# Performance work log

Measured on AMD Instinct MI355X. Metric: run time of the kernel, lower is better.

The kernel has to match this reference:

```python
import jax, jax.numpy as jnp
import numpy as np


def lrelu(x):
    return jax.nn.leaky_relu(x, 0.1)


def mask_softmax(a, mask, axis=-1):
    # faithful to the torch version: max over ALL entries, mask applied post-exp
    a_max = jnp.max(a, axis=axis, keepdims=True)
    e = jnp.exp(a - a_max) * mask
    return e / (jnp.sum(e, axis=axis, keepdims=True) + 1e-6)


def gru_cell(x, h, w_ih, w_hh, b_ih, b_hh):
    # torch.nn.GRUCell math; weights stored as [in, 3H]
    gi = x @ w_ih + b_ih
    gh = h @ w_hh + b_hh
    ir, iz, inn = jnp.split(gi, 3, axis=-1)
    hr, hz, hn = jnp.split(gh, 3, axis=-1)
    r = jax.nn.sigmoid(ir + hr)
    z = jax.nn.sigmoid(iz + hz)
    n = jnp.tanh(inn + r * hn)
    return (1 - z) * n + z * h


def setup_inputs() -> dict:
    key = jax.random.key(0)
    B, N, M, E, H, D, K = 128, 256, 12, 256, 128, 3, 2
    AF, BF, NA, NB = 82, 6, 100, 12
    ks = iter(jax.random.split(key, 64))
    nrm = lambda shape: jax.random.normal(next(ks), shape, jnp.float32) * 0.05
    return dict(
        batch_size=B,
        vertex_mask=jnp.ones((B, N), jnp.float32),
        vertex=jax.random.randint(next(ks), (B, N), 0, NA, dtype=jnp.int32),
        edge=jax.random.randint(next(ks), (B, E), 0, NB, dtype=jnp.int32),
        atom_adj=jax.random.randint(next(ks), (B * N * M,), 0, B * N, dtype=jnp.int32),
        bond_adj=jax.random.randint(next(ks), (B * N * M,), 0, B * E, dtype=jnp.int32),
        nbs_mask=jnp.ones((B, N, M), jnp.float32),
        init_atom_features=nrm((NA, AF)),
        init_bond_features=nrm((NB, BF)),
        emb_w=nrm((AF, H)), emb_b=nrm((H,)),
        Wa_main_w=nrm((D, K, H, H)), Wa_main_b=nrm((D, K, H)),
        Wbmm_w=nrm((D, K, H)), Wbmm_b=nrm((D, K)),
        Wmain_w=nrm((D, K, H, H)), Wmain_b=nrm((D, K, H)),
        Wm2s_w=nrm((D, K * H, H)), Wm2s_b=nrm((D, H)),
        Ws2m_w=nrm((D, H, H)), Ws2m_b=nrm((D, H)),
        Wsuper_w=nrm((D, H, H)), Wsuper_b=nrm((D, H)),
        Wzm1_w=nrm((D, H, H)), Wzm1_b=nrm((D, H)),
        Wzm2_w=nrm((D, H, H)), Wzm2_b=nrm((D, H)),
        Wzs1_w=nrm((D, H, H)), Wzs1_b=nrm((D, H)),
        Wzs2_w=nrm((D, H, H)), Wzs2_b=nrm((D, H)),
        U2_w=nrm((D, H + BF, H)), U2_b=nrm((D, H)),
        U1_w=nrm((D, 2 * H, H)), U1_b=nrm((D, H)),
        gm_wih=nrm((H, 3 * H)), gm_whh=nrm((H, 3 * H)), gm_bih=nrm((3 * H,)), gm_bhh=nrm((3 * H,)),
        gs_wih=nrm((H, 3 * H)), gs_whh=nrm((H, 3 * H)), gs_bih=nrm((3 * H,)), gs_bhh=nrm((3 * H,)),
    )


def reference(batch_size, vertex_mask, vertex, edge, atom_adj, bond_adj, nbs_mask,
              init_atom_features, init_bond_features, emb_w, emb_b,
              Wa_main_w, Wa_main_b, Wbmm_w, Wbmm_b, Wmain_w, Wmain_b,
              Wm2s_w, Wm2s_b, Ws2m_w, Ws2m_b, Wsuper_w, Wsuper_b,
              Wzm1_w, Wzm1_b, Wzm2_w, Wzm2_b, Wzs1_w, Wzs1_b, Wzs2_w, Wzs2_b,
              U2_w, U2_b, U1_w, U1_b,
              gm_wih, gm_whh, gm_bih, gm_bhh, gs_wih, gs_whh, gs_bih, gs_bhh):
    B = batch_size
    N = vertex_mask.shape[1]
    M = nbs_mask.shape[2]
    H = emb_w.shape[1]
    BF = init_bond_features.shape[1]
    D, K = Wa_main_w.shape[0], Wa_main_w.shape[1]

    vertex_initial = init_atom_features[vertex]          # [B,N,AF]
    edge_initial = init_bond_features[edge]              # [B,E,BF]
    vf = lrelu(vertex_initial @ emb_w + emb_b)           # [B,N,H]
    vm = vertex_mask[:, :, None]
    sf = jnp.sum(vf * vm, axis=1, keepdims=True)         # [B,1,H] super node

    for d in range(D):
        # multi-head super-node attention (all k heads vectorized)
        a_main = jnp.tanh(jnp.einsum('bnh,khg->bkng', vf, Wa_main_w[d]) + Wa_main_b[d][None, :, None, :])
        a = jnp.einsum('bkng,kg->bkn', a_main * sf[:, None, :, :], Wbmm_w[d]) + Wbmm_b[d][None, :, None]
        attn = mask_softmax(a, vertex_mask[:, None, :])                  # [B,K,N]
        wv = jnp.einsum('bnh,khg->bkng', vf, Wmain_w[d]) + Wmain_b[d][None, :, None, :]
        m = jnp.einsum('bkn,bkng->bkg', attn, wv).reshape(B, 1, K * H)   # head-concat
        main_to_super = jnp.tanh(m @ Wm2s_w[d] + Wm2s_b[d])              # [B,1,H]

        # WLN unit: gather neighbor atom/bond features, fused MLP + masked sum
        vnei = vf.reshape(-1, H)[atom_adj].reshape(B, N, M, H)
        enei = edge_initial.reshape(-1, BF)[bond_adj].reshape(B, N, M, BF)
        nei = jnp.concatenate([vnei, enei], axis=-1)                     # [B,N,M,H+BF]
        nei_label = lrelu(nei @ U2_w[d] + U2_b[d])
        nei_label = jnp.sum(nei_label * nbs_mask[..., None], axis=-2)    # [B,N,H]
        main_self = lrelu(jnp.concatenate([vf, nei_label], axis=-1) @ U1_w[d] + U1_b[d])

        super_to_main = jnp.tanh(sf @ Ws2m_w[d] + Ws2m_b[d])
        super_self = jnp.tanh(sf @ Wsuper_w[d] + Wsuper_b[d])

        z_main = jax.nn.sigmoid(main_self @ Wzm1_w[d] + Wzm1_b[d]
                                + super_to_main @ Wzm2_w[d] + Wzm2_b[d])
        hidden_main = (1 - z_main) * main_self + z_main * super_to_main
        vf = gru_cell(hidden_main.reshape(-1, H), vf.reshape(-1, H),
                      gm_wih, gm_whh, gm_bih, gm_bhh).reshape(B, N, H)

        z_super = jax.nn.sigmoid(super_self @ Wzs1_w[d] + Wzs1_b[d]
                                 + main_to_super @ Wzs2_w[d] + Wzs2_b[d])
        hidden_super = (1 - z_super) * super_self + z_super * main_to_super
        sf = gru_cell(hidden_super.reshape(B, H), sf.reshape(B, H),
                      gs_wih, gs_whh, gs_bih, gs_bhh).reshape(B, 1, H)

    return (vf, sf)
```

## Files before the change

kernel.cpp:

```cpp
#include <hip/hip_runtime.h>

typedef unsigned short ushort_t;
typedef unsigned int uint_t;
typedef unsigned char uchar_t;
typedef __attribute__((ext_vector_type(8))) short short8;
typedef __attribute__((ext_vector_type(4))) float f32x4;
typedef __attribute__((ext_vector_type(2))) float f32x2;

#define B   128
#define Nv  256
#define Mn  12
#define Hd  128
#define Dd  3
#define Kk  2
#define AFd 82
#define BFd 6
#define BN  (B*Nv)

enum { EPI_NONE = 0, EPI_LRELU = 1 };

__device__ __forceinline__ float lrelu(float x) { return fmaxf(x, 0.1f * x); }
__device__ __forceinline__ float sigmoidf(float x) { return 1.f / (1.f + expf(-x)); }
__device__ __forceinline__ ushort_t f2b(float x) {
    uint_t u = __float_as_uint(x);
    return (ushort_t)((u + 0x7FFFu + ((u >> 16) & 1u)) >> 16);
}
__device__ __forceinline__ float b2f(ushort_t s) {
    return __uint_as_float(((uint_t)s) << 16);
}
__device__ __forceinline__ void b2f4(uint2 u, float* o) {
    o[0] = __uint_as_float((u.x & 0xFFFFu) << 16);
    o[1] = __uint_as_float(u.x & 0xFFFF0000u);
    o[2] = __uint_as_float((u.y & 0xFFFFu) << 16);
    o[3] = __uint_as_float(u.y & 0xFFFF0000u);
}
__device__ __forceinline__ uint_t pk2(float lo, float hi) {
    return (uint_t)f2b(lo) | ((uint_t)f2b(hi) << 16);
}
__device__ __forceinline__ float upk_lo(uint_t u) { return __uint_as_float((u & 0xFFFFu) << 16); }
__device__ __forceinline__ float upk_hi(uint_t u) { return __uint_as_float(u & 0xFFFF0000u); }
__device__ __forceinline__ uchar_t f2e8(float x) {
    return (uchar_t)(__builtin_amdgcn_cvt_pk_fp8_f32(x, 0.f, 0, false) & 0xFF);
}

struct PrepJob {
    const float* W;
    long sliceStride;
    int K, ldw, nPerSlice, Kspan, KpadRow, kDst, total, outOff, blockStart;
};
struct PrepJobs { PrepJob j[18]; int nJobs; };

__global__ __launch_bounds__(256) void k_prep_all(PrepJobs P, ushort_t* __restrict__ WT)
{
    int bid = blockIdx.x;
    int ji = 0;
    #pragma unroll 1
    while (ji + 1 < P.nJobs && P.j[ji + 1].blockStart <= bid) ++ji;
    const PrepJob J = P.j[ji];
    const int idx = (bid - J.blockStart) * 256 + threadIdx.x;
    if (idx >= J.total) return;
    const int n = idx / J.Kspan, k = idx % J.Kspan;
    const int slice = n / J.nPerSlice, nn = n % J.nPerSlice;
    float v = (k < J.K) ? J.W[(size_t)slice * J.sliceStride + (size_t)k * J.ldw + nn] : 0.f;
    WT[(size_t)J.outOff + (size_t)n * J.KpadRow + J.kDst + k] = f2b(v);
}

__global__ __launch_bounds__(256) void k_qtab(const float* __restrict__ init_bond,
                                              const float* __restrict__ U2w,
                                              ushort_t* __restrict__ qt)
{
    const int d = blockIdx.x;
    const float* W = U2w + (size_t)d * (Hd + BFd) * Hd + (size_t)Hd * Hd;
    ushort_t* q = qt + (size_t)d * 12 * Hd;
    for (int idx = threadIdx.x; idx < 12 * Hd; idx += 256) {
        const int j = idx >> 7, h = idx & 127;
        float s = 0.f;
        #pragma unroll
        for (int f = 0; f < BFd; ++f) s += init_bond[j * BFd + f] * W[f * Hd + h];
        q[idx] = f2b(s);
    }
}

template<int EPI, bool ABF, bool OBF>
__global__ __launch_bounds__(256) void mgemm(
    const void* __restrict__ A1v, int lda1, int K1,
    const int* __restrict__ rowidx,
    const ushort_t* __restrict__ Wt, int Kpad,
    const float* __restrict__ b1,
    void* __restrict__ outv, long ldo)
{
    const int t    = threadIdx.x;
    const int lane = t & 63;
    const int w    = t >> 6;
    const int wm   = w >> 1, wn = w & 1;
    const int lr   = lane & 15, lg = lane >> 4;
    const int row0 = blockIdx.x * 64;

    __shared__ ushort_t As[64 * 64];

    f32x4 acc[2][4];
    #pragma unroll
    for (int i = 0; i < 2; ++i)
        #pragma unroll
        for (int j = 0; j < 4; ++j)
            acc[i][j] = (f32x4){0.f, 0.f, 0.f, 0.f};

    const int r_st = t >> 2, q4 = t & 3;
    const int grow = row0 + r_st;
    const long arow = rowidx ? (long)rowidx[grow] : (long)grow;

    const int nck = Kpad >> 6;
    for (int ck = 0; ck < nck; ++ck) {
        if (ck) __syncthreads();
        {
            const int kb = ck * 64 + q4 * 16;
            union { ushort_t us[16]; uint4 qv[2]; } tmp;
            #pragma unroll
            for (int j = 0; j < 16; ++j) {
                const int kg = kb + j;
                ushort_t v = 0;
                if (kg < K1) {
                    if (ABF) v = ((const ushort_t*)A1v)[(size_t)arow * lda1 + kg];
                    else     v = f2b(((const float*)A1v)[(size_t)arow * lda1 + kg]);
                }
                tmp.us[j] = v;
            }
            #pragma unroll
            for (int j = 0; j < 2; ++j) {
                int byte = r_st * 128 + q4 * 32 + j * 16;
                byte ^= ((r_st & 7) << 4);
                *(uint4*)((char*)As + byte) = tmp.qv[j];
            }
        }
        __syncthreads();
        #pragma unroll
        for (int ks = 0; ks < 64; ks += 32) {
            short8 af[2], bfr[4];
            #pragma unroll
            for (int mf = 0; mf < 2; ++mf) {
                const int row = wm * 32 + mf * 16 + lr;
                int byte = row * 128 + (ks + lg * 8) * 2;
                byte ^= ((row & 7) << 4);
                af[mf] = *(const short8*)((const char*)As + byte);
            }
            #pragma unroll
            for (int nf = 0; nf < 4; ++nf) {
                const int col = wn * 64 + nf * 16 + lr;
                bfr[nf] = *(const short8*)(Wt + (size_t)col * Kpad + ck * 64 + ks + lg * 8);
            }
            #pragma unroll
            for (int mf = 0; mf < 2; ++mf)
                #pragma unroll
                for (int nf = 0; nf < 4; ++nf)
                    acc[mf][nf] = __builtin_amdgcn_mfma_f32_16x16x32_bf16(
                        af[mf], bfr[nf], acc[mf][nf], 0, 0, 0);
        }
    }

    #pragma unroll
    for (int mf = 0; mf < 2; ++mf) {
        #pragma unroll
        for (int nf = 0; nf < 4; ++nf) {
            const int c = wn * 64 + nf * 16 + lr;
            #pragma unroll
            for (int reg = 0; reg < 4; ++reg) {
                const int r = wm * 32 + mf * 16 + lg * 4 + reg;
                const size_t row = (size_t)row0 + r;
                float v = acc[mf][nf][reg];
                if (b1) v += b1[c];
                if constexpr (EPI == EPI_LRELU) v = lrelu(v);
                const size_t oidx = row * ldo + c;
                if (OBF) ((ushort_t*)outv)[oidx] = f2b(v);
                else     ((float*)outv)[oidx] = v;
            }
        }
    }
}

__global__ __launch_bounds__(256) void k_tdp(
    const ushort_t* __restrict__ vfb,
    const ushort_t* __restrict__ Wt,
    const float* __restrict__ waB,
    const float* __restrict__ u2B,
    const float* __restrict__ sf,
    const float* __restrict__ wbmmW,
    const float* __restrict__ wbmmB,
    float* __restrict__ a_out,
    uchar_t* __restrict__ Pout)
{
    const int t = threadIdx.x;
    const int lane = t & 63, w = t >> 6;
    const int wm = w >> 1, wn = w & 1;
    const int lr = lane & 15, lg = lane >> 4;
    const int row0 = blockIdx.x * 64;
    const int ky = blockIdx.y;
    const int b = row0 >> 8;

    __shared__ ushort_t As[64 * 128];
    __shared__ float EUs[128], EBb[128];
    __shared__ float red[64][2];

    {
        const int r_st = t >> 2, q4 = t & 3;
        const ushort_t* src = vfb + (size_t)(row0 + r_st) * Hd + q4 * 32;
        #pragma unroll
        for (int j = 0; j < 4; ++j) {
            uint4 v = ((const uint4*)src)[j];
            int byte = r_st * 256 + q4 * 64 + j * 16;
            byte ^= ((r_st & 7) << 4);
            *(uint4*)((char*)As + byte) = v;
        }
    }
    if (ky != 2 && t < 128) {
        EUs[t] = sf[b * Hd + t] * wbmmW[ky * Hd + t];
        EBb[t] = waB[ky * Hd + t];
    }
    __syncthreads();

    const ushort_t* Wty = Wt + (size_t)ky * 16384;

    f32x4 acc[2][4];
    #pragma unroll
    for (int i = 0; i < 2; ++i)
        #pragma unroll
        for (int j = 0; j < 4; ++j)
            acc[i][j] = (f32x4){0.f, 0.f, 0.f, 0.f};

    #pragma unroll
    for (int kk = 0; kk < 128; kk += 32) {
        short8 af[2], bfr[4];
        #pragma unroll
        for (int nf = 0; nf < 4; ++nf) {
            const int col = wn * 64 + nf * 16 + lr;
            bfr[nf] = *(const short8*)(Wty + (size_t)col * 128 + kk + lg * 8);
        }
        #pragma unroll
        for (int mf = 0; mf < 2; ++mf) {
            const int row = wm * 32 + mf * 16 + lr;
            int byte = row * 256 + (kk + lg * 8) * 2;
            byte ^= ((row & 7) << 4);
            af[mf] = *(const short8*)((const char*)As + byte);
        }
        #pragma unroll
        for (int mf = 0; mf < 2; ++mf)
            #pragma unroll
            for (int nf = 0; nf < 4; ++nf)
                acc[mf][nf] = __builtin_amdgcn_mfma_f32_16x16x32_bf16(
                    af[mf], bfr[nf], acc[mf][nf], 0, 0, 0);
    }

    if (ky == 2) {
        #pragma unroll
        for (int mf = 0; mf < 2; ++mf)
            #pragma unroll
            for (int nf = 0; nf < 4; ++nf) {
                const int c = wn * 64 + nf * 16 + lr;
                #pragma unroll
                for (int reg = 0; reg < 4; ++reg) {
                    const int r = wm * 32 + mf * 16 + lg * 4 + reg;
                    Pout[(size_t)(row0 + r) * Hd + c] = f2e8(acc[mf][nf][reg] + u2B[c]);
                }
            }
    } else {
        #pragma unroll
        for (int mf = 0; mf < 2; ++mf) {
            #pragma unroll
            for (int reg = 0; reg < 4; ++reg) {
                float p = 0.f;
                #pragma unroll
                for (int nf = 0; nf < 4; ++nf) {
                    const int c = wn * 64 + nf * 16 + lr;
                    p += tanhf(acc[mf][nf][reg] + EBb[c]) * EUs[c];
                }
                p += __shfl_xor(p, 1); p += __shfl_xor(p, 2);
                p += __shfl_xor(p, 4); p += __shfl_xor(p, 8);
                if (lr == 0) red[wm * 32 + mf * 16 + lg * 4 + reg][wn] = p;
            }
        }
        __syncthreads();
        if (t < 64) {
            const int gr = row0 + t;
            a_out[(size_t)(gr >> 8) * 512 + (size_t)ky * 256 + (gr & 255)] =
                red[t][0] + red[t][1] + wbmmB[ky];
        }
    }
}

__device__ __forceinline__ void gemv1(const float* __restrict__ W0, const float* __restrict__ x0,
                                      int ldw, int off, int K,
                                      float (*red)[8][32][4],
                                      float* __restrict__ y0, int t)
{
    const int gq = t & 31, hs = t >> 5;
    const int hn = K >> 3;
    f32x4 a0 = (f32x4){0.f,0.f,0.f,0.f};
    const float* Wp0 = W0 + off + (size_t)gq * 4;
    const int h0 = hs * hn;
    #pragma unroll 8
    for (int i = 0; i < hn; ++i) {
        const float4 w0 = *(const float4*)&Wp0[(size_t)(h0 + i) * ldw];
        const float v0 = x0[h0 + i];
        a0.x = fmaf(v0, w0.x, a0.x); a0.y = fmaf(v0, w0.y, a0.y);
        a0.z = fmaf(v0, w0.z, a0.z); a0.w = fmaf(v0, w0.w, a0.w);
    }
    *(f32x4*)&red[0][hs][gq][0] = a0;
    __syncthreads();
    if (t < 128) {
        float s0 = 0.f;
        #pragma unroll
        for (int p = 0; p < 8; ++p) s0 += red[0][p][t >> 2][t & 3];
        y0[t] = s0;
    }
    __syncthreads();
}

__device__ __forceinline__ void gemv2(const float* __restrict__ W0, const float* __restrict__ x0,
                                      const float* __restrict__ W1, const float* __restrict__ x1,
                                      int ldw, int off, int K,
                                      float (*red)[8][32][4],
                                      float* __restrict__ y0, float* __restrict__ y1, int t)
{
    const int gq = t & 31, hs = t >> 5;
    const int hn = K >> 3;
    f32x4 a0 = (f32x4){0.f,0.f,0.f,0.f}, a1 = (f32x4){0.f,0.f,0.f,0.f};
    const float* Wp0 = W0 + off + (size_t)gq * 4;
    const float* Wp1 = W1 + off + (size_t)gq * 4;
    const int h0 = hs * hn;
    #pragma unroll 4
    for (int i = 0; i < hn; ++i) {
        const float4 w0 = *(const float4*)&Wp0[(size_t)(h0 + i) * ldw];
        const float4 w1 = *(const float4*)&Wp1[(size_t)(h0 + i) * ldw];
        const float v0 = x0[h0 + i], v1 = x1[h0 + i];
        a0.x = fmaf(v0, w0.x, a0.x); a0.y = fmaf(v0, w0.y, a0.y);
        a0.z = fmaf(v0, w0.z, a0.z); a0.w = fmaf(v0, w0.w, a0.w);
        a1.x = fmaf(v1, w1.x, a1.x); a1.y = fmaf(v1, w1.y, a1.y);
        a1.z = fmaf(v1, w1.z, a1.z); a1.w = fmaf(v1, w1.w, a1.w);
    }
    *(f32x4*)&red[0][hs][gq][0] = a0;
    *(f32x4*)&red[1][hs][gq][0] = a1;
    __syncthreads();
    if (t < 128) {
        float s0 = 0.f, s1 = 0.f;
        #pragma unroll
        for (int p = 0; p < 8; ++p) {
            s0 += red[0][p][t >> 2][t & 3];
            s1 += red[1][p][t >> 2][t & 3];
        }
        y0[t] = s0; y1[t] = s1;
    }
    __syncthreads();
}

__device__ __forceinline__ void gemv3(const float* __restrict__ W0, const float* __restrict__ x0,
                                      const float* __restrict__ W1, const float* __restrict__ x1,
                                      const float* __restrict__ W2, const float* __restrict__ x2,
                                      int ldw, int off, int K,
                                      float (*red)[8][32][4],
                                      float* __restrict__ y0, float* __restrict__ y1,
                                      float* __restrict__ y2, int t)
{
    const int gq = t & 31, hs = t >> 5;
    const int hn = K >> 3;
    f32x4 a0 = (f32x4){0.f,0.f,0.f,0.f}, a1 = (f32x4){0.f,0.f,0.f,0.f}, a2 = (f32x4){0.f,0.f,0.f,0.f};
    const float* Wp0 = W0 + off + (size_t)gq * 4;
    const float* Wp1 = W1 + off + (size_t)gq * 4;
    const float* Wp2 = W2 + off + (size_t)gq * 4;
    const int h0 = hs * hn;
    #pragma unroll 4
    for (int i = 0; i < hn; ++i) {
        const float4 w0 = *(const float4*)&Wp0[(size_t)(h0 + i) * ldw];
        const float4 w1 = *(const float4*)&Wp1[(size_t)(h0 + i) * ldw];
        const float4 w2 = *(const float4*)&Wp2[(size_t)(h0 + i) * ldw];
        const float v0 = x0[h0 + i], v1 = x1[h0 + i], v2 = x2[h0 + i];
        a0.x = fmaf(v0, w0.x, a0.x); a0.y = fmaf(v0, w0.y, a0.y);
        a0.z = fmaf(v0, w0.z, a0.z); a0.w = fmaf(v0, w0.w, a0.w);
        a1.x = fmaf(v1, w1.x, a1.x); a1.y = fmaf(v1, w1.y, a1.y);
        a1.z = fmaf(v1, w1.z, a1.z); a1.w = fmaf(v1, w1.w, a1.w);
        a2.x = fmaf(v2, w2.x, a2.x); a2.y = fmaf(v2, w2.y, a2.y);
        a2.z = fmaf(v2, w2.z, a2.z); a2.w = fmaf(v2, w2.w, a2.w);
    }
    *(f32x4*)&red[0][hs][gq][0] = a0;
    *(f32x4*)&red[1][hs][gq][0] = a1;
    *(f32x4*)&red[2][hs][gq][0] = a2;
    __syncthreads();
    if (t < 128) {
        float s0 = 0.f, s1 = 0.f, s2 = 0.f;
        #pragma unroll
        for (int p = 0; p < 8; ++p) {
            s0 += red[0][p][t >> 2][t & 3];
            s1 += red[1][p][t >> 2][t & 3];
            s2 += red[2][p][t >> 2][t & 3];
        }
        y0[t] = s0; y1[t] = s1; y2[t] = s2;
    }
    __syncthreads();
}

__global__ __launch_bounds__(256) void k_gsup(
    const float* __restrict__ a_buf, const float* __restrict__ vmask,
    const ushort_t* __restrict__ vfb,
    const float* __restrict__ sf_in,
    const float* __restrict__ Wm, const float* __restrict__ bm,
    const float* __restrict__ Wm2s, const float* __restrict__ bm2s,
    const float* __restrict__ Ws2m, const float* __restrict__ bs2m,
    const float* __restrict__ Wsup, const float* __restrict__ bsup,
    const float* __restrict__ Wzm2, const float* __restrict__ bzm2,
    const float* __restrict__ Wzs1, const float* __restrict__ bzs1,
    const float* __restrict__ Wzs2, const float* __restrict__ bzs2,
    const float* __restrict__ gwih, const float* __restrict__ gwhh,
    const float* __restrict__ gbih, const float* __restrict__ gbhh,
    float* __restrict__ s2m_g, float* __restrict__ czm2_g,
    float* __restrict__ sf_out,
    const uchar_t* __restrict__ P8, const ushort_t* __restrict__ qt,
    const int* __restrict__ aadj, const int* __restrict__ badj,
    const int* __restrict__ edge, const float* __restrict__ nmask,
    ushort_t* __restrict__ nei)
{
    const int t = threadIdx.x;

    if (blockIdx.x >= B) {
        __shared__ ushort_t aiS[64 * Mn];
        __shared__ ushort_t eiS[64 * Mn];
        __shared__ ushort_t mkS[64 * Mn];
        const int row0 = (blockIdx.x - B) * 64;
        for (int i = t; i < 64 * Mn; i += 256) {
            const int r = i / Mn, m = i - r * Mn;
            const long g = (long)(row0 + r) * Mn + m;
            aiS[i] = (ushort_t)aadj[g];
            eiS[i] = (ushort_t)edge[badj[g]];
            mkS[i] = f2b(nmask[g]);
        }
        __syncthreads();
        #pragma unroll 1
        for (int it = 0; it < 4; ++it) {
            const int idx = it * 256 + t;
            const int r = idx >> 4, h0 = (idx & 15) * 8;
            float a8[8] = {0.f,0.f,0.f,0.f,0.f,0.f,0.f,0.f};
            #pragma unroll
            for (int m = 0; m < Mn; ++m) {
                const int ai = aiS[r * Mn + m];
                const float mk = b2f(mkS[r * Mn + m]);
                const uint2 pv = *(const uint2*)&P8[(size_t)ai * Hd + h0];
                const uint4 qv = *(const uint4*)&qt[(size_t)eiS[r * Mn + m] * Hd + h0];
                const f32x2 p01 = __builtin_amdgcn_cvt_pk_f32_fp8((int)pv.x, false);
                const f32x2 p23 = __builtin_amdgcn_cvt_pk_f32_fp8((int)pv.x, true);
                const f32x2 p45 = __builtin_amdgcn_cvt_pk_f32_fp8((int)pv.y, false);
                const f32x2 p67 = __builtin_amdgcn_cvt_pk_f32_fp8((int)pv.y, true);
                const float pf[8] = {p01[0], p01[1], p23[0], p23[1], p45[0], p45[1], p67[0], p67[1]};
                const ushort_t* qq = (const ushort_t*)&qv;
                #pragma unroll
                for (int e = 0; e < 8; ++e) {
                    const float v = pf[e] + b2f(qq[e]);
                    a8[e] = fmaf(mk, lrelu(v), a8[e]);
                }
            }
            ushort_t o8[8];
            #pragma unroll
            for (int e = 0; e < 8; ++e) o8[e] = f2b(a8[e]);
            *(uint4*)&nei[(size_t)(row0 + r) * Hd + h0] = *(const uint4*)o8;
        }
        return;
    }

    const int b = blockIdx.x;
    const int wid = t >> 6, lane = t & 63;
    __shared__ float red[3][8][32][4];
    __shared__ float att0[256], att1[256];
    __shared__ float sfl[128], tbA[128], tbB[128], mv[256];
    __shared__ float ms2[128], s2ml[128], ssl[128], hsl[128];
    __shared__ float tmp1[128], tmp2[128], tmp3[128];
    __shared__ float gib[384], ghb[384];
    __shared__ float saS[2];
    __shared__ float lm[4][2], ls[4][2];

    const float v0 = a_buf[(size_t)b * 512 + t];
    const float v1 = a_buf[(size_t)b * 512 + 256 + t];
    const float vm = vmask[b * Nv + t];
    float m0 = v0, m1 = v1;
    #pragma unroll
    for (int o = 1; o < 64; o <<= 1) {
        m0 = fmaxf(m0, __shfl_xor(m0, o));
        m1 = fmaxf(m1, __shfl_xor(m1, o));
    }
    if (lane == 0) { lm[wid][0] = m0; lm[wid][1] = m1; }
    __syncthreads();
    m0 = fmaxf(fmaxf(lm[0][0], lm[1][0]), fmaxf(lm[2][0], lm[3][0]));
    m1 = fmaxf(fmaxf(lm[0][1], lm[1][1]), fmaxf(lm[2][1], lm[3][1]));
    const float e0v = expf(v0 - m0) * vm;
    const float e1v = expf(v1 - m1) * vm;
    float s0 = e0v, s1 = e1v;
    #pragma unroll
    for (int o = 1; o < 64; o <<= 1) {
        s0 += __shfl_xor(s0, o);
        s1 += __shfl_xor(s1, o);
    }
    if (lane == 0) { ls[wid][0] = s0; ls[wid][1] = s1; }
    if (t < 128) sfl[t] = sf_in[b * Hd + t];
    __syncthreads();
    s0 = ls[0][0] + ls[1][0] + ls[2][0] + ls[3][0];
    s1 = ls[0][1] + ls[1][1] + ls[2][1] + ls[3][1];
    att0[t] = e0v / (s0 + 1e-6f);
    att1[t] = e1v / (s1 + 1e-6f);
    if (t == 0) { saS[0] = s0 / (s0 + 1e-6f); saS[1] = s1 / (s1 + 1e-6f); }
    __syncthreads();

    {
        const int hq = t & 31, ns = t >> 5;
        f32x4 a0 = (f32x4){0.f,0.f,0.f,0.f}, a1 = (f32x4){0.f,0.f,0.f,0.f};
        const ushort_t* base = vfb + (size_t)b * Nv * Hd + hq * 4;
        #pragma unroll 8
        for (int i = 0; i < 32; ++i) {
            const int n = ns * 32 + i;
            float xv[4];
            b2f4(*(const uint2*)&base[(size_t)n * Hd], xv);
            const float w0 = att0[n], w1 = att1[n];
            a0.x = fmaf(w0, xv[0], a0.x); a0.y = fmaf(w0, xv[1], a0.y);
            a0.z = fmaf(w0, xv[2], a0.z); a0.w = fmaf(w0, xv[3], a0.w);
            a1.x = fmaf(w1, xv[0], a1.x); a1.y = fmaf(w1, xv[1], a1.y);
            a1.z = fmaf(w1, xv[2], a1.z); a1.w = fmaf(w1, xv[3], a1.w);
        }
        *(f32x4*)&red[0][ns][hq][0] = a0;
        *(f32x4*)&red[1][ns][hq][0] = a1;
        __syncthreads();
        if (t < 128) {
            float u0 = 0.f, u1 = 0.f;
            #pragma unroll
            for (int p = 0; p < 8; ++p) {
                u0 += red[0][p][t >> 2][t & 3];
                u1 += red[1][p][t >> 2][t & 3];
            }
            tbA[t] = u0; tbB[t] = u1;
        }
        __syncthreads();
    }

    gemv2(Wm, tbA, Wm + Hd * Hd, tbB, Hd, 0, Hd, red, mv, mv + 128, t);
    mv[t] += saS[t >> 7] * bm[t];
    __syncthreads();

    gemv1(Wm2s, mv, Hd, 0, 2 * Hd, red, tmp1, t);
    if (t < 128) ms2[t] = tanhf(tmp1[t] + bm2s[t]);
    __syncthreads();

    gemv2(Ws2m, sfl, Wsup, sfl, Hd, 0, Hd, red, tmp1, tmp2, t);
    if (t < 128) {
        const float v = tanhf(tmp1[t] + bs2m[t]);
        s2ml[t] = v; s2m_g[b * Hd + t] = v;
        ssl[t] = tanhf(tmp2[t] + bsup[t]);
    }
    __syncthreads();

    gemv3(Wzm2, s2ml, Wzs1, ssl, Wzs2, ms2, Hd, 0, Hd, red, tmp1, tmp2, tmp3, t);
    if (t < 128) {
        czm2_g[b * Hd + t] = tmp1[t] + bzm2[t];
        const float zs = sigmoidf(tmp2[t] + bzs1[t] + tmp3[t] + bzs2[t]);
        hsl[t] = (1.f - zs) * ssl[t] + zs * ms2[t];
    }
    __syncthreads();

    #pragma unroll 1
    for (int c = 0; c < 3; ++c)
        gemv2(gwih, hsl, gwhh, sfl, 3 * Hd, c * Hd, Hd, red, gib + c * Hd, ghb + c * Hd, t);
    if (t < 128) {
        const float r = sigmoidf(gib[t] + gbih[t] + ghb[t] + gbhh[t]);
        const float z = sigmoidf(gib[128 + t] + gbih[128 + t] + ghb[128 + t] + gbhh[128 + t]);
        const float n = tanhf(gib[256 + t] + gbih[256 + t] + r * (ghb[256 + t] + gbhh[256 + t]));
        sf_out[b * Hd + t] = (1.f - z) * n + z * sfl[t];
    }
}

__global__ __launch_bounds__(256) void k_mega(
    const ushort_t* __restrict__ vfb,
    const ushort_t* __restrict__ nei,
    const ushort_t* __restrict__ wt_u1,
    const ushort_t* __restrict__ wt_zm1,
    const ushort_t* __restrict__ wt_rz,
    const ushort_t* __restrict__ wt_inn,
    const ushort_t* __restrict__ wt_hn,
    const float* __restrict__ u1b,
    const float* __restrict__ zm1b,
    const float* __restrict__ bih, const float* __restrict__ bhh,
    const float* __restrict__ czm2, const float* __restrict__ s2m,
    void* __restrict__ outv, const int finalFp32)
{
    const int t = threadIdx.x;
    const int lane = t & 63;
    const int wn = t >> 6;
    const int lr = lane & 15, lg = lane >> 4;
    const int row0 = blockIdx.x * 32;
    const int b = row0 >> 8;

    __shared__ ushort_t As[32 * 256];

    {
        const int r_st = t >> 3, q8 = t & 7;
        const ushort_t* srcV = vfb + (size_t)(row0 + r_st) * Hd + q8 * 16;
        const ushort_t* srcN = nei + (size_t)(row0 + r_st) * Hd + q8 * 16;
        uint4 v0 = ((const uint4*)srcV)[0];
        uint4 v1 = ((const uint4*)srcV)[1];
        uint4 n0 = ((const uint4*)srcN)[0];
        uint4 n1 = ((const uint4*)srcN)[1];
        int bV0 = (r_st * 512 + q8 * 32)            ^ ((r_st & 7) << 4);
        int bV1 = (r_st * 512 + q8 * 32 + 16)       ^ ((r_st & 7) << 4);
        int bN0 = (r_st * 512 + 256 + q8 * 32)      ^ ((r_st & 7) << 4);
        int bN1 = (r_st * 512 + 256 + q8 * 32 + 16) ^ ((r_st & 7) << 4);
        *(uint4*)((char*)As + bV0) = v0;
        *(uint4*)((char*)As + bV1) = v1;
        *(uint4*)((char*)As + bN0) = n0;
        *(uint4*)((char*)As + bN1) = n1;
    }
    __syncthreads();

    f32x4 acc[2][2];

#define ZERO_ACC2() { _Pragma("unroll") for (int i = 0; i < 2; ++i) _Pragma("unroll") for (int j = 0; j < 2; ++j) acc[i][j] = (f32x4){0.f,0.f,0.f,0.f}; }
#define AF_L32(LC) (*(const short8*)((const char*)As + ((((mf * 16 + lr) * 512 + ((LC) + lg * 8) * 2)) ^ ((lr & 7) << 4))))
#define GEMM_PASS32(WG, KPADW, KTOT, A_EXPR) { \
        ZERO_ACC2(); \
        _Pragma("unroll") \
        for (int kk = 0; kk < (KTOT); kk += 32) { \
            short8 af[2], bfv[2]; \
            _Pragma("unroll") \
            for (int nf = 0; nf < 2; ++nf) \
                bfv[nf] = *(const short8*)((WG) + (size_t)(wn * 32 + nf * 16 + lr) * (KPADW) + kk + lg * 8); \
            _Pragma("unroll") \
            for (int mf = 0; mf < 2; ++mf) \
                af[mf] = (A_EXPR); \
            _Pragma("unroll") \
            for (int mf = 0; mf < 2; ++mf) \
                _Pragma("unroll") \
                for (int nf = 0; nf < 2; ++nf) \
                    acc[mf][nf] = __builtin_amdgcn_mfma_f32_16x16x32_bf16(af[mf], bfv[nf], acc[mf][nf], 0, 0, 0); \
        } }

    GEMM_PASS32(wt_u1, 256, 256, AF_L32(kk));
    {
        uint_t msp[2][2][2];
        #pragma unroll
        for (int mf = 0; mf < 2; ++mf)
            #pragma unroll
            for (int nf = 0; nf < 2; ++nf) {
                const int c = wn * 32 + nf * 16 + lr;
                const float bb = u1b[c];
                msp[mf][nf][0] = pk2(lrelu(acc[mf][nf][0] + bb), lrelu(acc[mf][nf][1] + bb));
                msp[mf][nf][1] = pk2(lrelu(acc[mf][nf][2] + bb), lrelu(acc[mf][nf][3] + bb));
            }
        __syncthreads();
        #pragma unroll
        for (int mf = 0; mf < 2; ++mf)
            #pragma unroll
            for (int nf = 0; nf < 2; ++nf) {
                const int c = wn * 32 + nf * 16 + lr;
                #pragma unroll
                for (int reg = 0; reg < 4; ++reg) {
                    const int row = mf * 16 + lg * 4 + reg;
                    const uint_t pk = msp[mf][nf][reg >> 1];
                    const ushort_t msb = (reg & 1) ? (ushort_t)(pk >> 16) : (ushort_t)(pk & 0xFFFFu);
                    int byte = row * 512 + (128 + c) * 2;
                    byte ^= ((row & 7) << 4);
                    *(ushort_t*)((char*)As + byte) = msb;
                }
            }
    }
    __syncthreads();

    GEMM_PASS32(wt_zm1, 128, 128, AF_L32(128 + kk));
    {
        uint_t zpk[2][2][2];
        #pragma unroll
        for (int mf = 0; mf < 2; ++mf)
            #pragma unroll
            for (int nf = 0; nf < 2; ++nf) {
                const int c = wn * 32 + nf * 16 + lr;
                const float bb = zm1b[c] + czm2[b * Hd + c];
                zpk[mf][nf][0] = pk2(sigmoidf(acc[mf][nf][0] + bb), sigmoidf(acc[mf][nf][1] + bb));
                zpk[mf][nf][1] = pk2(sigmoidf(acc[mf][nf][2] + bb), sigmoidf(acc[mf][nf][3] + bb));
            }
        __syncthreads();
        #pragma unroll
        for (int mf = 0; mf < 2; ++mf)
            #pragma unroll
            for (int nf = 0; nf < 2; ++nf) {
                const int c = wn * 32 + nf * 16 + lr;
                const float s2 = s2m[b * Hd + c];
                #pragma unroll
                for (int reg = 0; reg < 4; ++reg) {
                    const int row = mf * 16 + lg * 4 + reg;
                    int byte = row * 512 + (128 + c) * 2;
                    byte ^= ((row & 7) << 4);
                    const float ms = b2f(*(const ushort_t*)((const char*)As + byte));
                    const uint_t zp = zpk[mf][nf][reg >> 1];
                    const float z  = (reg & 1) ? upk_hi(zp) : upk_lo(zp);
                    *(ushort_t*)((char*)As + byte) = f2b((1.f - z) * ms + z * s2);
                }
            }
    }
    __syncthreads();

    uint_t innp[2][2][2], hnp[2][2][2];
    GEMM_PASS32(wt_inn, 128, 128, AF_L32(128 + kk));
    #pragma unroll
    for (int mf = 0; mf < 2; ++mf)
        #pragma unroll
        for (int nf = 0; nf < 2; ++nf) {
            const int c = wn * 32 + nf * 16 + lr;
            const float bb = bih[256 + c];
            innp[mf][nf][0] = pk2(acc[mf][nf][0] + bb, acc[mf][nf][1] + bb);
            innp[mf][nf][1] = pk2(acc[mf][nf][2] + bb, acc[mf][nf][3] + bb);
        }
    GEMM_PASS32(wt_hn, 128, 128, AF_L32(kk));
    #pragma unroll
    for (int mf = 0; mf < 2; ++mf)
        #pragma unroll
        for (int nf = 0; nf < 2; ++nf) {
            const int c = wn * 32 + nf * 16 + lr;
            const float bb = bhh[256 + c];
            hnp[mf][nf][0] = pk2(acc[mf][nf][0] + bb, acc[mf][nf][1] + bb);
            hnp[mf][nf][1] = pk2(acc[mf][nf][2] + bb, acc[mf][nf][3] + bb);
        }
    GEMM_PASS32(wt_rz, 256, 256, (kk < 128) ? AF_L32(128 + kk) : AF_L32(kk - 128));
    #pragma unroll
    for (int mf = 0; mf < 2; ++mf)
        #pragma unroll
        for (int nf = 0; nf < 2; ++nf) {
            const int c = wn * 32 + nf * 16 + lr;
            const float bb = bih[c] + bhh[c];
            const float r0 = sigmoidf(acc[mf][nf][0] + bb);
            const float r1 = sigmoidf(acc[mf][nf][1] + bb);
            const float r2 = sigmoidf(acc[mf][nf][2] + bb);
            const float r3 = sigmoidf(acc[mf][nf][3] + bb);
            const float n0 = tanhf(upk_lo(innp[mf][nf][0]) + r0 * upk_lo(hnp[mf][nf][0]));
            const float n1 = tanhf(upk_hi(innp[mf][nf][0]) + r1 * upk_hi(hnp[mf][nf][0]));
            const float n2 = tanhf(upk_lo(innp[mf][nf][1]) + r2 * upk_lo(hnp[mf][nf][1]));
            const float n3 = tanhf(upk_hi(innp[mf][nf][1]) + r3 * upk_hi(hnp[mf][nf][1]));
            innp[mf][nf][0] = pk2(n0, n1);
            innp[mf][nf][1] = pk2(n2, n3);
        }
    GEMM_PASS32(wt_rz + 128 * 256, 256, 256, (kk < 128) ? AF_L32(128 + kk) : AF_L32(kk - 128));
    #pragma unroll
    for (int mf = 0; mf < 2; ++mf)
        #pragma unroll
        for (int nf = 0; nf < 2; ++nf) {
            const int c = wn * 32 + nf * 16 + lr;
            const float bb = bih[128 + c] + bhh[128 + c];
            #pragma unroll
            for (int reg = 0; reg < 4; ++reg) {
                const int rl = mf * 16 + lg * 4 + reg;
                const float z = sigmoidf(acc[mf][nf][reg] + bb);
                const uint_t np = innp[mf][nf][reg >> 1];
                const float n = (reg & 1) ? upk_hi(np) : upk_lo(np);
                int byte = (rl * 512 + c * 2) ^ ((rl & 7) << 4);
                const float h = b2f(*(const ushort_t*)((const char*)As + byte));
                const float o = (1.f - z) * n + z * h;
                const size_t oidx = (size_t)(row0 + rl) * Hd + c;
                if (finalFp32) ((float*)outv)[oidx] = o;
                else           ((ushort_t*)outv)[oidx] = f2b(o);
            }
        }
#undef GEMM_PASS32
#undef ZERO_ACC2
#undef AF_L32
}

__global__ __launch_bounds__(256) void k_sfv(const ushort_t* __restrict__ vfb,
                                             const float* __restrict__ vmask,
                                             float* __restrict__ sf)
{
    const int b = blockIdx.x, t = threadIdx.x;
    __shared__ float vm[256];
    __shared__ float red[8][32][4];
    vm[t] = vmask[b * Nv + t];
    __syncthreads();
    const int hq = t & 31, ns = t >> 5;
    f32x4 acc = (f32x4){0.f,0.f,0.f,0.f};
    const ushort_t* base = vfb + (size_t)b * Nv * Hd + hq * 4;
    #pragma unroll 8
    for (int i = 0; i < 32; ++i) {
        const int n = ns * 32 + i;
        float xv[4];
        b2f4(*(const uint2*)&base[(size_t)n * Hd], xv);
        const float w = vm[n];
        acc.x = fmaf(w, xv[0], acc.x); acc.y = fmaf(w, xv[1], acc.y);
        acc.z = fmaf(w, xv[2], acc.z); acc.w = fmaf(w, xv[3], acc.w);
    }
    *(f32x4*)&red[ns][hq][0] = acc;
    __syncthreads();
    if (t < 128) {
        float s = 0.f;
        #pragma unroll
        for (int p = 0; p < 8; ++p) s += red[p][t >> 2][t & 3];
        sf[b * Hd + t] = s;
    }
}

extern "C" void kernel_launch(void* const* d_in, const int* in_sizes, int n_in,
                              void* d_out, int out_size, void* d_ws, size_t ws_size,
                              hipStream_t stream)
{
    (void)in_sizes; (void)n_in; (void)out_size;

    const float* vertex_mask = (const float*)d_in[1];
    const int*   vertex      = (const int*)d_in[2];
    const int*   edge        = (const int*)d_in[3];
    const int*   atom_adj    = (const int*)d_in[4];
    const int*   bond_adj    = (const int*)d_in[5];
    const float* nbs_mask    = (const float*)d_in[6];
    const float* init_atom   = (const float*)d_in[7];
    const float* init_bond   = (const float*)d_in[8];
    const float* emb_w  = (const float*)d_in[9];
    const float* emb_b  = (const float*)d_in[10];
    const float* Wa_w   = (const float*)d_in[11];
    const float* Wa_b   = (const float*)d_in[12];
    const float* Wbmm_w = (const float*)d_in[13];
    const float* Wbmm_b = (const float*)d_in[14];
    const float* Wm_w   = (const float*)d_in[15];
    const float* Wm_b   = (const float*)d_in[16];
    const float* Wm2s_w = (const float*)d_in[17];
    const float* Wm2s_b = (const float*)d_in[18];
    const float* Ws2m_w = (const float*)d_in[19];
    const float* Ws2m_b = (const float*)d_in[20];
    const float* Wsup_w = (const float*)d_in[21];
    const float* Wsup_b = (const float*)d_in[22];
    const float* Wzm1_w = (const float*)d_in[23];
    const float* Wzm1_b = (const float*)d_in[24];
    const float* Wzm2_w = (const float*)d_in[25];
    const float* Wzm2_b = (const float*)d_in[26];
    const float* Wzs1_w = (const float*)d_in[27];
    const float* Wzs1_b = (const float*)d_in[28];
    const float* Wzs2_w = (const float*)d_in[29];
    const float* Wzs2_b = (const float*)d_in[30];
    const float* U2_w   = (const float*)d_in[31];
    const float* U2_b   = (const float*)d_in[32];
    const float* U1_w   = (const float*)d_in[33];
    const float* U1_b   = (const float*)d_in[34];
    const float* gm_wih = (const float*)d_in[35];
    const float* gm_whh = (const float*)d_in[36];
    const float* gm_bih = (const float*)d_in[37];
    const float* gm_bhh = (const float*)d_in[38];
    const float* gs_wih = (const float*)d_in[39];
    const float* gs_whh = (const float*)d_in[40];
    const float* gs_bih = (const float*)d_in[41];
    const float* gs_bhh = (const float*)d_in[42];

    const size_t MB = 1u << 20;
    if (ws_size < 40 * MB) return;

    char* base = (char*)d_ws;
    ushort_t* VF0 = (ushort_t*)base;
    ushort_t* VF1 = (ushort_t*)(base + 8 * MB);
    uchar_t*  P8  = (uchar_t*)(base + 16 * MB);
    ushort_t* NEI = (ushort_t*)(base + 20 * MB);
    ushort_t* WT  = (ushort_t*)(base + 28 * MB);
    ushort_t* QT  = (ushort_t*)(base + 30 * MB);
    float*    S   = (float*)(base + 31 * MB);

    float* sfA    = S;
    float* sfB    = S + 16384;
    float* a_buf  = S + 32768;
    float* s2m    = S + 98304;
    float* c_zm2  = S + 114688;

    float* X1 = (float*)d_out;
    float* sf_final = X1 + (size_t)BN * Hd;

    const int OFF_EMB = 0;
    const int PERD = 98304;
    const int OFF_L0 = 16384;
    const int OFF_RZ = OFF_L0 + 3 * PERD;
    const int OFF_NH = OFF_RZ + 65536;

    PrepJobs PJ;
    int nj = 0, blk0 = 0;
    auto addJob = [&](const float* W, int K, int ldw, long sStride, int nPer,
                      int Kspan, int KpadRow, int kDst, int ncols, int outOff) {
        PrepJob& J = PJ.j[nj++];
        J.W = W; J.K = K; J.ldw = ldw; J.sliceStride = sStride; J.nPerSlice = nPer;
        J.Kspan = Kspan; J.KpadRow = KpadRow; J.kDst = kDst;
        J.total = ncols * Kspan; J.outOff = outOff; J.blockStart = blk0;
        blk0 += (J.total + 255) / 256;
    };
    addJob(emb_w, AFd, Hd, 0, Hd, 128, 128, 0, 128, OFF_EMB);
    for (int d = 0; d < Dd; ++d) {
        const int o = OFF_L0 + d * PERD;
        addJob(Wa_w + (long)d * Kk * Hd * Hd, Hd, Hd, (long)Hd * Hd, Hd, 128, 128, 0, 256, o);
        addJob(U2_w + (long)d * (Hd + BFd) * Hd, Hd, Hd, 0, Hd, 128, 128, 0, 128, o + 32768);
        addJob(U1_w + (long)d * 2 * Hd * Hd, 2 * Hd, Hd, 0, Hd, 256, 256, 0, 128, o + 49152);
        addJob(Wzm1_w + (long)d * Hd * Hd, Hd, Hd, 0, Hd, 128, 128, 0, 128, o + 81920);
    }
    addJob(gm_wih, Hd, 3 * Hd, 0, 256, 128, 256, 0,   256, OFF_RZ);
    addJob(gm_whh, Hd, 3 * Hd, 0, 256, 128, 256, 128, 256, OFF_RZ);
    addJob(gm_wih + 256, Hd, 3 * Hd, 0, 128, 128, 128, 0, 128, OFF_NH);
    addJob(gm_whh + 256, Hd, 3 * Hd, 0, 128, 128, 128, 0, 128, OFF_NH + 16384);
    PJ.nJobs = nj;
    k_prep_all<<<dim3(blk0), dim3(256), 0, stream>>>(PJ, WT);
    k_qtab<<<dim3(Dd), dim3(256), 0, stream>>>(init_bond, U2_w, QT);

    const dim3 blk(256);
    const dim3 g1(BN / 64, 1);
    const dim3 g32(BN / 32, 1);

    mgemm<EPI_LRELU, false, true><<<g1, blk, 0, stream>>>(
        init_atom, AFd, AFd, vertex,
        WT + OFF_EMB, 128, emb_b, VF0, Hd);
    k_sfv<<<dim3(B), blk, 0, stream>>>(VF0, vertex_mask, sfA);

    for (int d = 0; d < Dd; ++d) {
        ushort_t* vin  = (d & 1) ? VF1 : VF0;
        ushort_t* vout = (d & 1) ? VF0 : VF1;
        float* sin  = (d & 1) ? sfB : sfA;
        float* sout = (d == Dd - 1) ? sf_final : ((d & 1) ? sfA : sfB);

        const int o = OFF_L0 + d * PERD;

        k_tdp<<<dim3(BN / 64, 3), blk, 0, stream>>>(
            vin, WT + o,
            Wa_b + (long)d * Kk * Hd, U2_b + (long)d * Hd,
            sin, Wbmm_w + (long)d * Kk * Hd, Wbmm_b + (long)d * Kk,
            a_buf, P8);

        k_gsup<<<dim3(B + BN / 64), blk, 0, stream>>>(
            a_buf, vertex_mask, vin, sin,
            Wm_w + (long)d * Kk * Hd * Hd, Wm_b + (long)d * Kk * Hd,
            Wm2s_w + (long)d * Kk * Hd * Hd, Wm2s_b + (long)d * Hd,
            Ws2m_w + (long)d * Hd * Hd, Ws2m_b + (long)d * Hd,
            Wsup_w + (long)d * Hd * Hd, Wsup_b + (long)d * Hd,
            Wzm2_w + (long)d * Hd * Hd, Wzm2_b + (long)d * Hd,
            Wzs1_w + (long)d * Hd * Hd, Wzs1_b + (long)d * Hd,
            Wzs2_w + (long)d * Hd * Hd, Wzs2_b + (long)d * Hd,
            gs_wih, gs_whh, gs_bih, gs_bhh,
            s2m, c_zm2, sout,
            P8, QT + (size_t)d * 12 * Hd,
            atom_adj, bond_adj, edge, nbs_mask, NEI);

        k_mega<<<g32, blk, 0, stream>>>(
            vin, NEI,
            WT + o + 49152, WT + o + 81920,
            WT + OFF_RZ, WT + OFF_NH, WT + OFF_NH + 16384,
            U1_b + (long)d * Hd, Wzm1_b + (long)d * Hd,
            gm_bih, gm_bhh,
            c_zm2, s2m,
            (d == Dd - 1) ? (void*)X1 : (void*)vout, (d == Dd - 1) ? 1 : 0);
    }
}
```

Measured before the change: 305.9 us.

## Shrink k_mega row tile to 16 rows and fuse r/z gate GEMMs

Each k_mega block now processes 16 rows instead of 32, doubling the grid and halving shared memory per block, so more blocks can be resident and tail imbalance is reduced. The r and z GRU gate GEMMs are merged into one pass with four accumulators, so the A fragment is read from LDS once per k step for both gates. In exchange, each weight fragment is reused across only one row fragment instead of two, so global and L2 weight traffic per output row doubles.

```diff
diff --git a/kernel.cpp b/kernel.cpp
--- a/kernel.cpp
+++ b/kernel.cpp
@@ -587,179 +587,153 @@
     const int lane = t & 63;
     const int wn = t >> 6;
     const int lr = lane & 15, lg = lane >> 4;
-    const int row0 = blockIdx.x * 32;
+    const int row0 = blockIdx.x * 16;
     const int b = row0 >> 8;
 
-    __shared__ ushort_t As[32 * 256];
+    __shared__ ushort_t As[16 * 256];
 
     {
-        const int r_st = t >> 3, q8 = t & 7;
-        const ushort_t* srcV = vfb + (size_t)(row0 + r_st) * Hd + q8 * 16;
-        const ushort_t* srcN = nei + (size_t)(row0 + r_st) * Hd + q8 * 16;
-        uint4 v0 = ((const uint4*)srcV)[0];
-        uint4 v1 = ((const uint4*)srcV)[1];
-        uint4 n0 = ((const uint4*)srcN)[0];
-        uint4 n1 = ((const uint4*)srcN)[1];
-        int bV0 = (r_st * 512 + q8 * 32)            ^ ((r_st & 7) << 4);
-        int bV1 = (r_st * 512 + q8 * 32 + 16)       ^ ((r_st & 7) << 4);
-        int bN0 = (r_st * 512 + 256 + q8 * 32)      ^ ((r_st & 7) << 4);
-        int bN1 = (r_st * 512 + 256 + q8 * 32 + 16) ^ ((r_st & 7) << 4);
-        *(uint4*)((char*)As + bV0) = v0;
-        *(uint4*)((char*)As + bV1) = v1;
-        *(uint4*)((char*)As + bN0) = n0;
-        *(uint4*)((char*)As + bN1) = n1;
-    }
-    __syncthreads();
-
-    f32x4 acc[2][2];
-
-#define ZERO_ACC2() { _Pragma("unroll") for (int i = 0; i < 2; ++i) _Pragma("unroll") for (int j = 0; j < 2; ++j) acc[i][j] = (f32x4){0.f,0.f,0.f,0.f}; }
-#define AF_L32(LC) (*(const short8*)((const char*)As + ((((mf * 16 + lr) * 512 + ((LC) + lg * 8) * 2)) ^ ((lr & 7) << 4))))
-#define GEMM_PASS32(WG, KPADW, KTOT, A_EXPR) { \
-        ZERO_ACC2(); \
+        const int r_st = t >> 4, q16 = t & 15;
+        uint4 v = *(const uint4*)(vfb + (size_t)(row0 + r_st) * Hd + q16 * 8);
+        uint4 n = *(const uint4*)(nei + (size_t)(row0 + r_st) * Hd + q16 * 8);
+        int bV = (r_st * 512 + q16 * 16)       ^ ((r_st & 7) << 4);
+        int bN = (r_st * 512 + 256 + q16 * 16) ^ ((r_st & 7) << 4);
+        *(uint4*)((char*)As + bV) = v;
+        *(uint4*)((char*)As + bN) = n;
+    }
+    __syncthreads();
+
+#define AF16(LC) (*(const short8*)((const char*)As + (((lr * 512 + ((LC) + lg * 8) * 2)) ^ ((lr & 7) << 4))))
+
+    f32x4 acc2[2];
+    f32x4 acc4[4];
+
+#define GEMM_P2(WG, KPADW, KTOT, A_EXPR) { \
+        acc2[0] = (f32x4){0.f,0.f,0.f,0.f}; acc2[1] = (f32x4){0.f,0.f,0.f,0.f}; \
         _Pragma("unroll") \
         for (int kk = 0; kk < (KTOT); kk += 32) { \
-            short8 af[2], bfv[2]; \
+            short8 af = (A_EXPR); \
             _Pragma("unroll") \
-            for (int nf = 0; nf < 2; ++nf) \
-                bfv[nf] = *(const short8*)((WG) + (size_t)(wn * 32 + nf * 16 + lr) * (KPADW) + kk + lg * 8); \
-            _Pragma("unroll") \
-            for (int mf = 0; mf < 2; ++mf) \
-                af[mf] = (A_EXPR); \
-            _Pragma("unroll") \
-            for (int mf = 0; mf < 2; ++mf) \
-                _Pragma("unroll") \
-                for (int nf = 0; nf < 2; ++nf) \
-                    acc[mf][nf] = __builtin_amdgcn_mfma_f32_16x16x32_bf16(af[mf], bfv[nf], acc[mf][nf], 0, 0, 0); \
+            for (int nf = 0; nf < 2; ++nf) { \
+                short8 bfv = *(const short8*)((WG) + (size_t)(wn * 32 + nf * 16 + lr) * (KPADW) + kk + lg * 8); \
+                acc2[nf] = __builtin_amdgcn_mfma_f32_16x16x32_bf16(af, bfv, acc2[nf], 0, 0, 0); \
+            } \
         } }
 
-    GEMM_PASS32(wt_u1, 256, 256, AF_L32(kk));
+    GEMM_P2(wt_u1, 256, 256, AF16(kk));
     {
-        uint_t msp[2][2][2];
-        #pragma unroll
-        for (int mf = 0; mf < 2; ++mf)
-            #pragma unroll
-            for (int nf = 0; nf < 2; ++nf) {
-                const int c = wn * 32 + nf * 16 + lr;
-                const float bb = u1b[c];
-                msp[mf][nf][0] = pk2(lrelu(acc[mf][nf][0] + bb), lrelu(acc[mf][nf][1] + bb));
-                msp[mf][nf][1] = pk2(lrelu(acc[mf][nf][2] + bb), lrelu(acc[mf][nf][3] + bb));
-            }
-        __syncthreads();
-        #pragma unroll
-        for (int mf = 0; mf < 2; ++mf)
-            #pragma unroll
-            for (int nf = 0; nf < 2; ++nf) {
-                const int c = wn * 32 + nf * 16 + lr;
-                #pragma unroll
-                for (int reg = 0; reg < 4; ++reg) {
-                    const int row = mf * 16 + lg * 4 + reg;
-                    const uint_t pk = msp[mf][nf][reg >> 1];
-                    const ushort_t msb = (reg & 1) ? (ushort_t)(pk >> 16) : (ushort_t)(pk & 0xFFFFu);
-                    int byte = row * 512 + (128 + c) * 2;
-                    byte ^= ((row & 7) << 4);
-                    *(ushort_t*)((char*)As + byte) = msb;
-                }
-            }
-    }
-    __syncthreads();
-
-    GEMM_PASS32(wt_zm1, 128, 128, AF_L32(128 + kk));
-    {
-        uint_t zpk[2][2][2];
-        #pragma unroll
-        for (int mf = 0; mf < 2; ++mf)
-            #pragma unroll
-            for (int nf = 0; nf < 2; ++nf) {
-                const int c = wn * 32 + nf * 16 + lr;
-                const float bb = zm1b[c] + czm2[b * Hd + c];
-                zpk[mf][nf][0] = pk2(sigmoidf(acc[mf][nf][0] + bb), sigmoidf(acc[mf][nf][1] + bb));
-                zpk[mf][nf][1] = pk2(sigmoidf(acc[mf][nf][2] + bb), sigmoidf(acc[mf][nf][3] + bb));
-            }
-        __syncthreads();
-        #pragma unroll
-        for (int mf = 0; mf < 2; ++mf)
-            #pragma unroll
-            for (int nf = 0; nf < 2; ++nf) {
-                const int c = wn * 32 + nf * 16 + lr;
-                const float s2 = s2m[b * Hd + c];
-                #pragma unroll
-                for (int reg = 0; reg < 4; ++reg) {
-                    const int row = mf * 16 + lg * 4 + reg;
-                    int byte = row * 512 + (128 + c) * 2;
-                    byte ^= ((row & 7) << 4);
-                    const float ms = b2f(*(const ushort_t*)((const char*)As + byte));
-                    const uint_t zp = zpk[mf][nf][reg >> 1];
-                    const float z  = (reg & 1) ? upk_hi(zp) : upk_lo(zp);
-                    *(ushort_t*)((char*)As + byte) = f2b((1.f - z) * ms + z * s2);
-                }
-            }
-    }
-    __syncthreads();
-
-    uint_t innp[2][2][2], hnp[2][2][2];
-    GEMM_PASS32(wt_inn, 128, 128, AF_L32(128 + kk));
-    #pragma unroll
-    for (int mf = 0; mf < 2; ++mf)
+        uint_t msp[2][2];
         #pragma unroll
         for (int nf = 0; nf < 2; ++nf) {
             const int c = wn * 32 + nf * 16 + lr;
-            const float bb = bih[256 + c];
-            innp[mf][nf][0] = pk2(acc[mf][nf][0] + bb, acc[mf][nf][1] + bb);
-            innp[mf][nf][1] = pk2(acc[mf][nf][2] + bb, acc[mf][nf][3] + bb);
-        }
-    GEMM_PASS32(wt_hn, 128, 128, AF_L32(kk));
-    #pragma unroll
-    for (int mf = 0; mf < 2; ++mf)
+            const float bb = u1b[c];
+            msp[nf][0] = pk2(lrelu(acc2[nf][0] + bb), lrelu(acc2[nf][1] + bb));
+            msp[nf][1] = pk2(lrelu(acc2[nf][2] + bb), lrelu(acc2[nf][3] + bb));
+        }
+        __syncthreads();
         #pragma unroll
         for (int nf = 0; nf < 2; ++nf) {
             const int c = wn * 32 + nf * 16 + lr;
-            const float bb = bhh[256 + c];
-            hnp[mf][nf][0] = pk2(acc[mf][nf][0] + bb, acc[mf][nf][1] + bb);
-            hnp[mf][nf][1] = pk2(acc[mf][nf][2] + bb, acc[mf][nf][3] + bb);
-        }
-    GEMM_PASS32(wt_rz, 256, 256, (kk < 128) ? AF_L32(128 + kk) : AF_L32(kk - 128));
-    #pragma unroll
-    for (int mf = 0; mf < 2; ++mf)
+            #pragma unroll
+            for (int reg = 0; reg < 4; ++reg) {
+                const int row = lg * 4 + reg;
+                const uint_t pk = msp[nf][reg >> 1];
+                const ushort_t msb = (reg & 1) ? (ushort_t)(pk >> 16) : (ushort_t)(pk & 0xFFFFu);
+                int byte = row * 512 + (128 + c) * 2;
+                byte ^= ((row & 7) << 4);
+                *(ushort_t*)((char*)As + byte) = msb;
+            }
+        }
+    }
+    __syncthreads();
+
+    GEMM_P2(wt_zm1, 128, 128, AF16(128 + kk));
+    {
+        uint_t zpk[2][2];
         #pragma unroll
         for (int nf = 0; nf < 2; ++nf) {
             const int c = wn * 32 + nf * 16 + lr;
-            const float bb = bih[c] + bhh[c];
-            const float r0 = sigmoidf(acc[mf][nf][0] + bb);
-            const float r1 = sigmoidf(acc[mf][nf][1] + bb);
-            const float r2 = sigmoidf(acc[mf][nf][2] + bb);
-            const float r3 = sigmoidf(acc[mf][nf][3] + bb);
-            const float n0 = tanhf(upk_lo(innp[mf][nf][0]) + r0 * upk_lo(hnp[mf][nf][0]));
-            const float n1 = tanhf(upk_hi(innp[mf][nf][0]) + r1 * upk_hi(hnp[mf][nf][0]));
-            const float n2 = tanhf(upk_lo(innp[mf][nf][1]) + r2 * upk_lo(hnp[mf][nf][1]));
-            const float n3 = tanhf(upk_hi(innp[mf][nf][1]) + r3 * upk_hi(hnp[mf][nf][1]));
-            innp[mf][nf][0] = pk2(n0, n1);
-            innp[mf][nf][1] = pk2(n2, n3);
-        }
-    GEMM_PASS32(wt_rz + 128 * 256, 256, 256, (kk < 128) ? AF_L32(128 + kk) : AF_L32(kk - 128));
-    #pragma unroll
-    for (int mf = 0; mf < 2; ++mf)
+            const float bb = zm1b[c] + czm2[b * Hd + c];
+            zpk[nf][0] = pk2(sigmoidf(acc2[nf][0] + bb), sigmoidf(acc2[nf][1] + bb));
+            zpk[nf][1] = pk2(sigmoidf(acc2[nf][2] + bb), sigmoidf(acc2[nf][3] + bb));
+        }
+        __syncthreads();
         #pragma unroll
         for (int nf = 0; nf < 2; ++nf) {
             const int c = wn * 32 + nf * 16 + lr;
-            const float bb = bih[128 + c] + bhh[128 + c];
+            const float s2 = s2m[b * Hd + c];
             #pragma unroll
             for (int reg = 0; reg < 4; ++reg) {
-                const int rl = mf * 16 + lg * 4 + reg;
-                const float z = sigmoidf(acc[mf][nf][reg] + bb);
-                const uint_t np = innp[mf][nf][reg >> 1];
-                const float n = (reg & 1) ? upk_hi(np) : upk_lo(np);
-                int byte = (rl * 512 + c * 2) ^ ((rl & 7) << 4);
-                const float h = b2f(*(const ushort_t*)((const char*)As + byte));
-                const float o = (1.f - z) * n + z * h;
-                const size_t oidx = (size_t)(row0 + rl) * Hd + c;
-                if (finalFp32) ((float*)outv)[oidx] = o;
-                else           ((ushort_t*)outv)[oidx] = f2b(o);
-            }
-        }
-#undef GEMM_PASS32
-#undef ZERO_ACC2
-#undef AF_L32
+                const int row = lg * 4 + reg;
+                int byte = row * 512 + (128 + c) * 2;
+                byte ^= ((row & 7) << 4);
+                const float ms = b2f(*(const ushort_t*)((const char*)As + byte));
+                const uint_t zp = zpk[nf][reg >> 1];
+                const float z  = (reg & 1) ? upk_hi(zp) : upk_lo(zp);
+                *(ushort_t*)((char*)As + byte) = f2b((1.f - z) * ms + z * s2);
+            }
+        }
+    }
+    __syncthreads();
+
+    uint_t innp[2][2], hnp[2][2];
+    GEMM_P2(wt_inn, 128, 128, AF16(128 + kk));
+    #pragma unroll
+    for (int nf = 0; nf < 2; ++nf) {
+        const int c = wn * 32 + nf * 16 + lr;
+        const float bb = bih[256 + c];
+        innp[nf][0] = pk2(acc2[nf][0] + bb, acc2[nf][1] + bb);
+        innp[nf][1] = pk2(acc2[nf][2] + bb, acc2[nf][3] + bb);
+    }
+    GEMM_P2(wt_hn, 128, 128, AF16(kk));
+    #pragma unroll
+    for (int nf = 0; nf < 2; ++nf) {
+        const int c = wn * 32 + nf * 16 + lr;
+        const float bb = bhh[256 + c];
+        hnp[nf][0] = pk2(acc2[nf][0] + bb, acc2[nf][1] + bb);
+        hnp[nf][1] = pk2(acc2[nf][2] + bb, acc2[nf][3] + bb);
+    }
+
+    {
+        #pragma unroll
+        for (int i = 0; i < 4; ++i) acc4[i] = (f32x4){0.f,0.f,0.f,0.f};
+        #pragma unroll
+        for (int kk = 0; kk < 256; kk += 32) {
+            short8 af = (kk < 128) ? AF16(128 + kk) : AF16(kk - 128);
+            #pragma unroll
+            for (int nf = 0; nf < 4; ++nf) {
+                const int wcol = (nf < 2) ? (wn * 32 + nf * 16 + lr)
+                                          : (128 + wn * 32 + (nf - 2) * 16 + lr);
+                short8 bfv = *(const short8*)(wt_rz + (size_t)wcol * 256 + kk + lg * 8);
+                acc4[nf] = __builtin_amdgcn_mfma_f32_16x16x32_bf16(af, bfv, acc4[nf], 0, 0, 0);
+            }
+        }
+    }
+    #pragma unroll
+    for (int nf = 0; nf < 2; ++nf) {
+        const int c = wn * 32 + nf * 16 + lr;
+        const float bbr = bih[c] + bhh[c];
+        const float bbz = bih[128 + c] + bhh[128 + c];
+        #pragma unroll
+        for (int reg = 0; reg < 4; ++reg) {
+            const int rl = lg * 4 + reg;
+            const float r = sigmoidf(acc4[nf][reg] + bbr);
+            const float z = sigmoidf(acc4[nf + 2][reg] + bbz);
+            const uint_t ip = innp[nf][reg >> 1];
+            const uint_t hp = hnp[nf][reg >> 1];
+            const float inn = (reg & 1) ? upk_hi(ip) : upk_lo(ip);
+            const float hnv = (reg & 1) ? upk_hi(hp) : upk_lo(hp);
+            const float n = tanhf(inn + r * hnv);
+            int byte = (rl * 512 + c * 2) ^ ((rl & 7) << 4);
+            const float h = b2f(*(const ushort_t*)((const char*)As + byte));
+            const float o = (1.f - z) * n + z * h;
+            const size_t oidx = (size_t)(row0 + rl) * Hd + c;
+            if (finalFp32) ((float*)outv)[oidx] = o;
+            else           ((ushort_t*)outv)[oidx] = f2b(o);
+        }
+    }
+#undef GEMM_P2
+#undef AF16
 }
 
 __global__ __launch_bounds__(256) void k_sfv(const ushort_t* __restrict__ vfb,
@@ -897,7 +871,7 @@
 
     const dim3 blk(256);
     const dim3 g1(BN / 64, 1);
-    const dim3 g32(BN / 32, 1);
+    const dim3 g16(BN / 16, 1);
 
     mgemm<EPI_LRELU, false, true><<<g1, blk, 0, stream>>>(
         init_atom, AFd, AFd, vertex,
@@ -932,7 +906,7 @@
             P8, QT + (size_t)d * 12 * Hd,
             atom_adj, bond_adj, edge, nbs_mask, NEI);
 
-        k_mega<<<g32, blk, 0, stream>>>(
+        k_mega<<<g16, blk, 0, stream>>>(
             vin, NEI,
             WT + o + 49152, WT + o + 81920,
             WT + OFF_RZ, WT + OFF_NH, WT + OFF_NH + 16384,
```

Result: slower. 379.9 us (+24.2%).
